# Performance work log

Hardware: AMD Instinct MI355X
Metric: run time of the kernel (lower is better)

## Reference

```python
import jax, jax.numpy as jnp
import numpy as np

N_INPUTS = 1024
N_MIDDLE = 256
N_OUTPUTS = 64
BATCH = 65536


def setup_inputs() -> dict:
    key = jax.random.key(0)
    k_x, k_w1, k_w2 = jax.random.split(key, 3)
    x = jax.random.normal(k_x, (BATCH, N_INPUTS), dtype=jnp.float32)
    # Synapse weights k are initialized with random.random() in [0, 1)
    W1 = jax.random.uniform(k_w1, (N_MIDDLE, N_INPUTS), dtype=jnp.float32)
    W2 = jax.random.uniform(k_w2, (N_OUTPUTS, N_MIDDLE), dtype=jnp.float32)
    # Neuron biases b are initialized to 0.0
    b1 = jnp.zeros((N_MIDDLE,), dtype=jnp.float32)
    b2 = jnp.zeros((N_OUTPUTS,), dtype=jnp.float32)
    return {"x": x, "W1": W1, "b1": b1, "W2": W2, "b2": b2}


def reference(x, W1, b1, W2, b2):
    # Middle RegularNeurons: relu(sum_j k_ij * x_j + b_i)
    h = jax.nn.relu(jnp.einsum('bi,mi->bm', x, W1) + b1)  # [B, n_middle]
    # Output DestinationNeurons: relu(sum_m k_om * h_m + b_o)
    y = jax.nn.relu(jnp.einsum('bm,om->bo', h, W2) + b2)  # [B, n_outputs]
    return y
```

## Files before the change

### kernel.cpp

```cpp
#include <hip/hip_runtime.h>
#include <stdint.h>

#define NIN 1024
#define NMID 256
#define NOUT 64
#define BM 128
#define BK 64

typedef __attribute__((ext_vector_type(8))) short bf16x8;
typedef __attribute__((ext_vector_type(4))) float fx4;
typedef __attribute__((ext_vector_type(16))) float f32x16;
typedef __attribute__((ext_vector_type(4))) uint32_t u32x4;

#define XS_TILE 32768
#define LDS_SZ  65536

union FragU { bf16x8 v; uint32_t u[4]; };

static __device__ __forceinline__ uint32_t cvtpk(float lo, float hi) {
  uint32_t r;
  asm("v_cvt_pk_bf16_f32 %0, %1, %2" : "=v"(r) : "v"(lo), "v"(hi));
  return r;
}
static __device__ __forceinline__ void gload16(const void* g, void* l) {
  __builtin_amdgcn_global_load_lds(
      (const __attribute__((address_space(1))) uint32_t*)g,
      (__attribute__((address_space(3))) uint32_t*)l, 16, 0, 0);
}

__global__ __launch_bounds__(256) void cvt_weights(
    const float* __restrict__ W1, const float* __restrict__ W2,
    unsigned short* __restrict__ w1f, unsigned short* __restrict__ w2b) {
  int gid = blockIdx.x * 256 + threadIdx.x;
  if (gid < 32768) {
    int r = gid & 31;
    int kb = (gid >> 5) & 127;
    int c = gid >> 12;
    const float* s = W1 + (size_t)(c * 32 + r) * NIN + kb * 8;
    fx4 v0 = *(const fx4*)s;
    fx4 v1 = *(const fx4*)(s + 4);
    u32x4 o = {cvtpk(v0.x, v0.y), cvtpk(v0.z, v0.w),
               cvtpk(v1.x, v1.y), cvtpk(v1.z, v1.w)};
    *(u32x4*)(w1f + (size_t)gid * 8) = o;
  } else {
    int e2 = (gid - 32768) << 2;
    if (e2 < NOUT * NMID) {
      fx4 v = *(const fx4*)(W2 + e2);
      uint2 p; p.x = cvtpk(v.x, v.y); p.y = cvtpk(v.z, v.w);
      *(uint2*)(w2b + e2) = p;
    }
  }
}

__global__ __launch_bounds__(512, 4) void livenet_main(
    const float* __restrict__ x,
    const unsigned short* __restrict__ w1f,
    const float* __restrict__ b1,
    const unsigned short* __restrict__ w2b,
    const float* __restrict__ b2,
    float* __restrict__ y) {

  extern __shared__ __align__(16) char smem[];

  const int tid = threadIdx.x;
  const int lane = tid & 63;
  const int w = tid >> 6;
  const int wm = w >> 2;
  const int wn = w & 3;
  const int l31 = lane & 31;
  const int l15 = lane & 15;
  const int lh = lane >> 5;
  const int row0 = blockIdx.x * BM;

  uint32_t xsrc[4], xdst[4];
#pragma unroll
  for (int i = 0; i < 4; ++i) {
    uint32_t o = (uint32_t)(i * 8192 + tid * 16);
    uint32_t r = o >> 8;
    uint32_t pc = (o >> 4) & 15u;
    uint32_t j = pc ^ (r & 15u);
    xsrc[i] = (uint32_t)(row0 + (int)r) * NIN + j * 4u;
    xdst[i] = o;
  }

#define XSTAGE(pbuf, k0)                                        \
  { char* xb_ = smem + (pbuf) * XS_TILE;                        \
    _Pragma("unroll") for (int i_ = 0; i_ < 4; ++i_)            \
      gload16(x + xsrc[i_] + (k0), xb_ + xdst[i_]); }

  f32x16 acc[2][2];
#pragma unroll
  for (int mt = 0; mt < 2; ++mt)
#pragma unroll
    for (int nt = 0; nt < 2; ++nt)
#pragma unroll
      for (int q = 0; q < 16; ++q) acc[mt][nt][q] = 0.f;

  const unsigned short* wf0 = w1f + ((size_t)(wn * 2 + 0) * 4096 + l31) * 8;
  const unsigned short* wf1 = w1f + ((size_t)(wn * 2 + 1) * 4096 + l31) * 8;

  const uint32_t ar0 = (uint32_t)(wm * 64 + l31) * 256u;
  const uint32_t ar1 = (uint32_t)(wm * 64 + 32 + l31) * 256u;

  XSTAGE(0, 0);
  __syncthreads();

  for (int t = 0; t < 16; ++t) {
    const int pc = t & 1;
    const char* xb = smem + pc * XS_TILE;

    bf16x8 bfr[2][4];
#pragma unroll
    for (int kk = 0; kk < 4; ++kk) {
      uint32_t kb = (uint32_t)(t * 8 + kk * 2 + lh);
      bfr[0][kk] = *(const bf16x8*)(wf0 + kb * 256u);
      bfr[1][kk] = *(const bf16x8*)(wf1 + kb * 256u);
    }

    if (t < 15) XSTAGE(pc ^ 1, (t + 1) * BK);

#pragma unroll
    for (int kk = 0; kk < 4; ++kk) {
      bf16x8 a0, a1;
      {
        uint32_t j0 = (uint32_t)(kk * 4 + lh * 2);
        fx4 va = *(const fx4*)(xb + ar0 + ((j0 ^ (uint32_t)l15) << 4));
        fx4 vb = *(const fx4*)(xb + ar0 + (((j0 + 1) ^ (uint32_t)l15) << 4));
        FragU f;
        f.u[0] = cvtpk(va.x, va.y); f.u[1] = cvtpk(va.z, va.w);
        f.u[2] = cvtpk(vb.x, vb.y); f.u[3] = cvtpk(vb.z, vb.w);
        a0 = f.v;
        fx4 vc = *(const fx4*)(xb + ar1 + ((j0 ^ (uint32_t)l15) << 4));
        fx4 vd = *(const fx4*)(xb + ar1 + (((j0 + 1) ^ (uint32_t)l15) << 4));
        FragU g;
        g.u[0] = cvtpk(vc.x, vc.y); g.u[1] = cvtpk(vc.z, vc.w);
        g.u[2] = cvtpk(vd.x, vd.y); g.u[3] = cvtpk(vd.z, vd.w);
        a1 = g.v;
      }
      __builtin_amdgcn_s_setprio(1);
      acc[0][0] = __builtin_amdgcn_mfma_f32_32x32x16_bf16(a0, bfr[0][kk], acc[0][0], 0, 0, 0);
      acc[0][1] = __builtin_amdgcn_mfma_f32_32x32x16_bf16(a0, bfr[1][kk], acc[0][1], 0, 0, 0);
      acc[1][0] = __builtin_amdgcn_mfma_f32_32x32x16_bf16(a1, bfr[0][kk], acc[1][0], 0, 0, 0);
      acc[1][1] = __builtin_amdgcn_mfma_f32_32x32x16_bf16(a1, bfr[1][kk], acc[1][1], 0, 0, 0);
      __builtin_amdgcn_s_setprio(0);
    }
    __syncthreads();
  }

  float b1v[2];
#pragma unroll
  for (int nt = 0; nt < 2; ++nt) b1v[nt] = b1[wn * 64 + nt * 32 + l31];

#pragma unroll
  for (int mt = 0; mt < 2; ++mt) {
#pragma unroll
    for (int nt = 0; nt < 2; ++nt) {
      int col = wn * 64 + nt * 32 + l31;
#pragma unroll
      for (int rg = 0; rg < 16; ++rg) {
        int row = wm * 64 + mt * 32 + (rg & 3) + 8 * (rg >> 2) + 4 * lh;
        float v = acc[mt][nt][rg] + b1v[nt];
        v = v > 0.f ? v : 0.f;
        int j = (col >> 3) ^ (row & 31);
        *(unsigned short*)(smem + row * 512 + (j << 4) + (col & 7) * 2) =
            (unsigned short)cvtpk(v, v);
      }
    }
  }
  __syncthreads();

  f32x16 acc2;
#pragma unroll
  for (int q = 0; q < 16; ++q) acc2[q] = 0.f;

  const int r2 = (w >> 1) * 32;
  const int c2 = (w & 1) * 32;
  const int arow = r2 + l31;
  const uint32_t arx = (uint32_t)(arow & 31);
  const unsigned short* w2row = w2b + (size_t)(c2 + l31) * NMID + lh * 8;

#pragma unroll
  for (int kk = 0; kk < 16; ++kk) {
    bf16x8 a2 = *(const bf16x8*)(smem + arow * 512 +
                                 ((((uint32_t)(kk * 2 + lh)) ^ arx) << 4));
    bf16x8 bw = *(const bf16x8*)(w2row + kk * 16);
    acc2 = __builtin_amdgcn_mfma_f32_32x32x16_bf16(a2, bw, acc2, 0, 0, 0);
  }

  float bias2 = b2[c2 + l31];
#pragma unroll
  for (int rg = 0; rg < 16; ++rg) {
    int row = r2 + (rg & 3) + 8 * (rg >> 2) + 4 * lh;
    float v = acc2[rg] + bias2;
    v = v > 0.f ? v : 0.f;
    y[(size_t)(row0 + row) * NOUT + c2 + l31] = v;
  }
}

extern "C" void kernel_launch(void* const* d_in, const int* in_sizes, int n_in,
                              void* d_out, int out_size, void* d_ws, size_t ws_size,
                              hipStream_t stream) {
  const float* x  = (const float*)d_in[0];
  const float* W1 = (const float*)d_in[1];
  const float* b1 = (const float*)d_in[2];
  const float* W2 = (const float*)d_in[3];
  const float* b2 = (const float*)d_in[4];
  float* y = (float*)d_out;

  unsigned short* w1f = (unsigned short*)d_ws;
  unsigned short* w2b = w1f + (size_t)NMID * NIN;

  const int batch = in_sizes[0] / NIN;

  hipLaunchKernelGGL(cvt_weights, dim3(144), dim3(256), 0, stream,
                     W1, W2, w1f, w2b);

  static int lds_set = 0;
  if (!lds_set) {
    hipFuncSetAttribute((const void*)livenet_main,
                        hipFuncAttributeMaxDynamicSharedMemorySize, LDS_SZ);
    lds_set = 1;
  }
  hipLaunchKernelGGL(livenet_main, dim3(batch / BM), dim3(512), LDS_SZ, stream,
                     x, w1f, b1, w2b, b2, y);
}
```

Measured before the change: 89.19 us.

## Load x directly from global into MFMA fragments, dropping LDS staging

Removes the double-buffered global-to-LDS staging of x. Each wave now reads its x fragments straight from global memory, converts them to bf16 and feeds the MFMAs. The block shrinks to 64 rows and 4 waves, with static 32KB LDS used only for the hidden activations. This drops LDS round trips and per-tile barriers, but every wave reloads the same x rows, so L1/L2 traffic rises. The row-strided per-lane loads coalesce less well and lose explicit prefetch overlap.

```diff
diff --git a/kernel.cpp b/kernel.cpp
--- a/kernel.cpp
+++ b/kernel.cpp
@@ -4,16 +4,12 @@
 #define NIN 1024
 #define NMID 256
 #define NOUT 64
-#define BM 128
-#define BK 64
+#define BM 64
 
 typedef __attribute__((ext_vector_type(8))) short bf16x8;
 typedef __attribute__((ext_vector_type(4))) float fx4;
 typedef __attribute__((ext_vector_type(16))) float f32x16;
 typedef __attribute__((ext_vector_type(4))) uint32_t u32x4;
-
-#define XS_TILE 32768
-#define LDS_SZ  65536
 
 union FragU { bf16x8 v; uint32_t u[4]; };
 
@@ -21,11 +17,6 @@
   uint32_t r;
   asm("v_cvt_pk_bf16_f32 %0, %1, %2" : "=v"(r) : "v"(lo), "v"(hi));
   return r;
-}
-static __device__ __forceinline__ void gload16(const void* g, void* l) {
-  __builtin_amdgcn_global_load_lds(
-      (const __attribute__((address_space(1))) uint32_t*)g,
-      (__attribute__((address_space(3))) uint32_t*)l, 16, 0, 0);
 }
 
 __global__ __launch_bounds__(256) void cvt_weights(
@@ -52,7 +43,7 @@
   }
 }
 
-__global__ __launch_bounds__(512, 4) void livenet_main(
+__global__ __launch_bounds__(256, 3) void livenet_main(
     const float* __restrict__ x,
     const unsigned short* __restrict__ w1f,
     const float* __restrict__ b1,
@@ -60,33 +51,15 @@
     const float* __restrict__ b2,
     float* __restrict__ y) {
 
-  extern __shared__ __align__(16) char smem[];
+  __shared__ __align__(16) char smem[32768];
 
   const int tid = threadIdx.x;
   const int lane = tid & 63;
   const int w = tid >> 6;
-  const int wm = w >> 2;
-  const int wn = w & 3;
+  const int wn = w;
   const int l31 = lane & 31;
-  const int l15 = lane & 15;
   const int lh = lane >> 5;
   const int row0 = blockIdx.x * BM;
-
-  uint32_t xsrc[4], xdst[4];
-#pragma unroll
-  for (int i = 0; i < 4; ++i) {
-    uint32_t o = (uint32_t)(i * 8192 + tid * 16);
-    uint32_t r = o >> 8;
-    uint32_t pc = (o >> 4) & 15u;
-    uint32_t j = pc ^ (r & 15u);
-    xsrc[i] = (uint32_t)(row0 + (int)r) * NIN + j * 4u;
-    xdst[i] = o;
-  }
-
-#define XSTAGE(pbuf, k0)                                        \
-  { char* xb_ = smem + (pbuf) * XS_TILE;                        \
-    _Pragma("unroll") for (int i_ = 0; i_ < 4; ++i_)            \
-      gload16(x + xsrc[i_] + (k0), xb_ + xdst[i_]); }
 
   f32x16 acc[2][2];
 #pragma unroll
@@ -99,16 +72,10 @@
   const unsigned short* wf0 = w1f + ((size_t)(wn * 2 + 0) * 4096 + l31) * 8;
   const unsigned short* wf1 = w1f + ((size_t)(wn * 2 + 1) * 4096 + l31) * 8;
 
-  const uint32_t ar0 = (uint32_t)(wm * 64 + l31) * 256u;
-  const uint32_t ar1 = (uint32_t)(wm * 64 + 32 + l31) * 256u;
-
-  XSTAGE(0, 0);
-  __syncthreads();
+  const float* xr0 = x + (size_t)(row0 + l31) * NIN;
+  const float* xr1 = x + (size_t)(row0 + 32 + l31) * NIN;
 
   for (int t = 0; t < 16; ++t) {
-    const int pc = t & 1;
-    const char* xb = smem + pc * XS_TILE;
-
     bf16x8 bfr[2][4];
 #pragma unroll
     for (int kk = 0; kk < 4; ++kk) {
@@ -117,34 +84,25 @@
       bfr[1][kk] = *(const bf16x8*)(wf1 + kb * 256u);
     }
 
-    if (t < 15) XSTAGE(pc ^ 1, (t + 1) * BK);
-
 #pragma unroll
     for (int kk = 0; kk < 4; ++kk) {
-      bf16x8 a0, a1;
-      {
-        uint32_t j0 = (uint32_t)(kk * 4 + lh * 2);
-        fx4 va = *(const fx4*)(xb + ar0 + ((j0 ^ (uint32_t)l15) << 4));
-        fx4 vb = *(const fx4*)(xb + ar0 + (((j0 + 1) ^ (uint32_t)l15) << 4));
-        FragU f;
-        f.u[0] = cvtpk(va.x, va.y); f.u[1] = cvtpk(va.z, va.w);
-        f.u[2] = cvtpk(vb.x, vb.y); f.u[3] = cvtpk(vb.z, vb.w);
-        a0 = f.v;
-        fx4 vc = *(const fx4*)(xb + ar1 + ((j0 ^ (uint32_t)l15) << 4));
-        fx4 vd = *(const fx4*)(xb + ar1 + (((j0 + 1) ^ (uint32_t)l15) << 4));
-        FragU g;
-        g.u[0] = cvtpk(vc.x, vc.y); g.u[1] = cvtpk(vc.z, vc.w);
-        g.u[2] = cvtpk(vd.x, vd.y); g.u[3] = cvtpk(vd.z, vd.w);
-        a1 = g.v;
-      }
+      const int kof = t * 64 + (kk * 2 + lh) * 8;
+      fx4 va = *(const fx4*)(xr0 + kof);
+      fx4 vb = *(const fx4*)(xr0 + kof + 4);
+      fx4 vc = *(const fx4*)(xr1 + kof);
+      fx4 vd = *(const fx4*)(xr1 + kof + 4);
+      FragU f, g;
+      f.u[0] = cvtpk(va.x, va.y); f.u[1] = cvtpk(va.z, va.w);
+      f.u[2] = cvtpk(vb.x, vb.y); f.u[3] = cvtpk(vb.z, vb.w);
+      g.u[0] = cvtpk(vc.x, vc.y); g.u[1] = cvtpk(vc.z, vc.w);
+      g.u[2] = cvtpk(vd.x, vd.y); g.u[3] = cvtpk(vd.z, vd.w);
       __builtin_amdgcn_s_setprio(1);
-      acc[0][0] = __builtin_amdgcn_mfma_f32_32x32x16_bf16(a0, bfr[0][kk], acc[0][0], 0, 0, 0);
-      acc[0][1] = __builtin_amdgcn_mfma_f32_32x32x16_bf16(a0, bfr[1][kk], acc[0][1], 0, 0, 0);
-      acc[1][0] = __builtin_amdgcn_mfma_f32_32x32x16_bf16(a1, bfr[0][kk], acc[1][0], 0, 0, 0);
-      acc[1][1] = __builtin_amdgcn_mfma_f32_32x32x16_bf16(a1, bfr[1][kk], acc[1][1], 0, 0, 0);
+      acc[0][0] = __builtin_amdgcn_mfma_f32_32x32x16_bf16(f.v, bfr[0][kk], acc[0][0], 0, 0, 0);
+      acc[0][1] = __builtin_amdgcn_mfma_f32_32x32x16_bf16(f.v, bfr[1][kk], acc[0][1], 0, 0, 0);
+      acc[1][0] = __builtin_amdgcn_mfma_f32_32x32x16_bf16(g.v, bfr[0][kk], acc[1][0], 0, 0, 0);
+      acc[1][1] = __builtin_amdgcn_mfma_f32_32x32x16_bf16(g.v, bfr[1][kk], acc[1][1], 0, 0, 0);
       __builtin_amdgcn_s_setprio(0);
     }
-    __syncthreads();
   }
 
   float b1v[2];
@@ -158,7 +116,7 @@
       int col = wn * 64 + nt * 32 + l31;
 #pragma unroll
       for (int rg = 0; rg < 16; ++rg) {
-        int row = wm * 64 + mt * 32 + (rg & 3) + 8 * (rg >> 2) + 4 * lh;
+        int row = mt * 32 + (rg & 3) + 8 * (rg >> 2) + 4 * lh;
         float v = acc[mt][nt][rg] + b1v[nt];
         v = v > 0.f ? v : 0.f;
         int j = (col >> 3) ^ (row & 31);
@@ -214,13 +172,6 @@
 
   hipLaunchKernelGGL(cvt_weights, dim3(144), dim3(256), 0, stream,
                      W1, W2, w1f, w2b);
-
-  static int lds_set = 0;
-  if (!lds_set) {
-    hipFuncSetAttribute((const void*)livenet_main,
-                        hipFuncAttributeMaxDynamicSharedMemorySize, LDS_SZ);
-    lds_set = 1;
-  }
-  hipLaunchKernelGGL(livenet_main, dim3(batch / BM), dim3(512), LDS_SZ, stream,
+  hipLaunchKernelGGL(livenet_main, dim3(batch / BM), dim3(256), 0, stream,
                      x, w1f, b1, w2b, b2, y);
 }
```

Result: slower. 160.1 us (+79.5%).

## Halve row tile and prefetch x two stages ahead with explicit vmcnt waits

Applied to the files above, without the earlier changes.

Shrinks the block to 64 rows and 4 waves of 256 threads, with 32KB of LDS and up to 3 blocks per CU. Each wave now covers all 64 rows for its column slice. The x staging now issues both buffers up front and refills a buffer two k-steps ahead. It uses explicit s_waitcnt vmcnt and lgkmcnt plus raw barriers in place of __syncthreads, so global loads stay in flight across the compute. The aim is better latency hiding and occupancy, but each block still reads all of W1, so L2 traffic for weights doubles.

```diff
diff --git a/kernel.cpp b/kernel.cpp
--- a/kernel.cpp
+++ b/kernel.cpp
@@ -4,7 +4,7 @@
 #define NIN 1024
 #define NMID 256
 #define NOUT 64
-#define BM 128
+#define BM 64
 #define BK 64
 
 typedef __attribute__((ext_vector_type(8))) short bf16x8;
@@ -12,8 +12,8 @@
 typedef __attribute__((ext_vector_type(16))) float f32x16;
 typedef __attribute__((ext_vector_type(4))) uint32_t u32x4;
 
-#define XS_TILE 32768
-#define LDS_SZ  65536
+#define XS_TILE 16384
+#define LDS_SZ  32768
 
 union FragU { bf16x8 v; uint32_t u[4]; };
 
@@ -27,6 +27,12 @@
       (const __attribute__((address_space(1))) uint32_t*)g,
       (__attribute__((address_space(3))) uint32_t*)l, 16, 0, 0);
 }
+
+#define VMCNT4() asm volatile("s_waitcnt vmcnt(4)" ::: "memory")
+#define VMCNT0() asm volatile("s_waitcnt vmcnt(0)" ::: "memory")
+#define LGKM0()  asm volatile("s_waitcnt lgkmcnt(0)" ::: "memory")
+#define SBAR()   __builtin_amdgcn_s_barrier()
+#define SFENCE() __builtin_amdgcn_sched_barrier(0)
 
 __global__ __launch_bounds__(256) void cvt_weights(
     const float* __restrict__ W1, const float* __restrict__ W2,
@@ -52,7 +58,7 @@
   }
 }
 
-__global__ __launch_bounds__(512, 4) void livenet_main(
+__global__ __launch_bounds__(256, 3) void livenet_main(
     const float* __restrict__ x,
     const unsigned short* __restrict__ w1f,
     const float* __restrict__ b1,
@@ -65,8 +71,7 @@
   const int tid = threadIdx.x;
   const int lane = tid & 63;
   const int w = tid >> 6;
-  const int wm = w >> 2;
-  const int wn = w & 3;
+  const int wn = w;
   const int l31 = lane & 31;
   const int l15 = lane & 15;
   const int lh = lane >> 5;
@@ -75,7 +80,7 @@
   uint32_t xsrc[4], xdst[4];
 #pragma unroll
   for (int i = 0; i < 4; ++i) {
-    uint32_t o = (uint32_t)(i * 8192 + tid * 16);
+    uint32_t o = (uint32_t)(i * 4096 + tid * 16);
     uint32_t r = o >> 8;
     uint32_t pc = (o >> 4) & 15u;
     uint32_t j = pc ^ (r & 15u);
@@ -99,15 +104,18 @@
   const unsigned short* wf0 = w1f + ((size_t)(wn * 2 + 0) * 4096 + l31) * 8;
   const unsigned short* wf1 = w1f + ((size_t)(wn * 2 + 1) * 4096 + l31) * 8;
 
-  const uint32_t ar0 = (uint32_t)(wm * 64 + l31) * 256u;
-  const uint32_t ar1 = (uint32_t)(wm * 64 + 32 + l31) * 256u;
+  const uint32_t ar0 = (uint32_t)(l31) * 256u;
+  const uint32_t ar1 = (uint32_t)(32 + l31) * 256u;
 
   XSTAGE(0, 0);
-  __syncthreads();
+  XSTAGE(1, BK);
 
   for (int t = 0; t < 16; ++t) {
-    const int pc = t & 1;
-    const char* xb = smem + pc * XS_TILE;
+    if (t < 15) { VMCNT4(); } else { VMCNT0(); }
+    SBAR();
+    SFENCE();
+
+    const char* xb = smem + (t & 1) * XS_TILE;
 
     bf16x8 bfr[2][4];
 #pragma unroll
@@ -117,34 +125,30 @@
       bfr[1][kk] = *(const bf16x8*)(wf1 + kb * 256u);
     }
 
-    if (t < 15) XSTAGE(pc ^ 1, (t + 1) * BK);
-
 #pragma unroll
     for (int kk = 0; kk < 4; ++kk) {
-      bf16x8 a0, a1;
-      {
-        uint32_t j0 = (uint32_t)(kk * 4 + lh * 2);
-        fx4 va = *(const fx4*)(xb + ar0 + ((j0 ^ (uint32_t)l15) << 4));
-        fx4 vb = *(const fx4*)(xb + ar0 + (((j0 + 1) ^ (uint32_t)l15) << 4));
-        FragU f;
-        f.u[0] = cvtpk(va.x, va.y); f.u[1] = cvtpk(va.z, va.w);
-        f.u[2] = cvtpk(vb.x, vb.y); f.u[3] = cvtpk(vb.z, vb.w);
-        a0 = f.v;
-        fx4 vc = *(const fx4*)(xb + ar1 + ((j0 ^ (uint32_t)l15) << 4));
-        fx4 vd = *(const fx4*)(xb + ar1 + (((j0 + 1) ^ (uint32_t)l15) << 4));
-        FragU g;
-        g.u[0] = cvtpk(vc.x, vc.y); g.u[1] = cvtpk(vc.z, vc.w);
-        g.u[2] = cvtpk(vd.x, vd.y); g.u[3] = cvtpk(vd.z, vd.w);
-        a1 = g.v;
-      }
+      uint32_t j0 = (uint32_t)(kk * 4 + lh * 2);
+      fx4 va = *(const fx4*)(xb + ar0 + ((j0 ^ (uint32_t)l15) << 4));
+      fx4 vb = *(const fx4*)(xb + ar0 + (((j0 + 1) ^ (uint32_t)l15) << 4));
+      fx4 vc = *(const fx4*)(xb + ar1 + ((j0 ^ (uint32_t)l15) << 4));
+      fx4 vd = *(const fx4*)(xb + ar1 + (((j0 + 1) ^ (uint32_t)l15) << 4));
+      FragU f, g;
+      f.u[0] = cvtpk(va.x, va.y); f.u[1] = cvtpk(va.z, va.w);
+      f.u[2] = cvtpk(vb.x, vb.y); f.u[3] = cvtpk(vb.z, vb.w);
+      g.u[0] = cvtpk(vc.x, vc.y); g.u[1] = cvtpk(vc.z, vc.w);
+      g.u[2] = cvtpk(vd.x, vd.y); g.u[3] = cvtpk(vd.z, vd.w);
       __builtin_amdgcn_s_setprio(1);
-      acc[0][0] = __builtin_amdgcn_mfma_f32_32x32x16_bf16(a0, bfr[0][kk], acc[0][0], 0, 0, 0);
-      acc[0][1] = __builtin_amdgcn_mfma_f32_32x32x16_bf16(a0, bfr[1][kk], acc[0][1], 0, 0, 0);
-      acc[1][0] = __builtin_amdgcn_mfma_f32_32x32x16_bf16(a1, bfr[0][kk], acc[1][0], 0, 0, 0);
-      acc[1][1] = __builtin_amdgcn_mfma_f32_32x32x16_bf16(a1, bfr[1][kk], acc[1][1], 0, 0, 0);
+      acc[0][0] = __builtin_amdgcn_mfma_f32_32x32x16_bf16(f.v, bfr[0][kk], acc[0][0], 0, 0, 0);
+      acc[0][1] = __builtin_amdgcn_mfma_f32_32x32x16_bf16(f.v, bfr[1][kk], acc[0][1], 0, 0, 0);
+      acc[1][0] = __builtin_amdgcn_mfma_f32_32x32x16_bf16(g.v, bfr[0][kk], acc[1][0], 0, 0, 0);
+      acc[1][1] = __builtin_amdgcn_mfma_f32_32x32x16_bf16(g.v, bfr[1][kk], acc[1][1], 0, 0, 0);
       __builtin_amdgcn_s_setprio(0);
     }
-    __syncthreads();
+
+    LGKM0();
+    SBAR();
+    SFENCE();
+    if (t + 2 < 16) XSTAGE(t & 1, (t + 2) * BK);
   }
 
   float b1v[2];
@@ -158,7 +162,7 @@
       int col = wn * 64 + nt * 32 + l31;
 #pragma unroll
       for (int rg = 0; rg < 16; ++rg) {
-        int row = wm * 64 + mt * 32 + (rg & 3) + 8 * (rg >> 2) + 4 * lh;
+        int row = mt * 32 + (rg & 3) + 8 * (rg >> 2) + 4 * lh;
         float v = acc[mt][nt][rg] + b1v[nt];
         v = v > 0.f ? v : 0.f;
         int j = (col >> 3) ^ (row & 31);
@@ -221,6 +225,6 @@
                         hipFuncAttributeMaxDynamicSharedMemorySize, LDS_SZ);
     lds_set = 1;
   }
-  hipLaunchKernelGGL(livenet_main, dim3(batch / BM), dim3(512), LDS_SZ, stream,
+  hipLaunchKernelGGL(livenet_main, dim3(batch / BM), dim3(256), LDS_SZ, stream,
                      x, w1f, b1, w2b, b2, y);
 }
```

New measurement: 82.90 us. -7.1%, faster.
